# Kernel optimization log

Measured on AMD Instinct MI355X. Metric: run time of the kernel, lower is better.

Reference implementation:

```python
import jax, jax.numpy as jnp
import numpy as np

N = 50000       # nodes per batched graph
E = 800000      # edges per batched graph
G = 256         # graphs per batch (for max-node pooling)
VOCAB = 120     # node types == embedding vocab
D_EMB = 32
D_H = 100
D_FC = 32
MIN_TYPE = 5    # min_type_count in compute_node_pair_mmd
CAP = 25        # max_nodes_per_type (deterministic: first CAP nodes per type)
KER_MUL = 2.0   # standard multi-kernel Gaussian MMD settings
KER_NUM = 5


def setup_inputs() -> dict:
    key = jax.random.key(0)
    ks = jax.random.split(key, 16)
    ri = lambda k, sh, hi: jax.random.randint(k, sh, 0, hi, dtype=jnp.int32)
    feat = ri(ks[0], (N,), VOCAB)
    feat_src = ri(ks[1], (N,), VOCAB)
    feat_tar = ri(ks[2], (N,), VOCAB)
    edge_index = ri(ks[3], (2, E), N)
    edge_index_src = ri(ks[4], (2, E), N)
    edge_index_tar = ri(ks[5], (2, E), N)
    graph_ids = (jnp.arange(N, dtype=jnp.int32) * G) // N  # sorted, even partition
    mask = (jax.random.uniform(ks[6], (N,)) > 0.1).astype(jnp.float32)
    embed = jax.random.normal(ks[7], (VOCAB, D_EMB)) * 0.02
    gcn_w = jax.random.normal(ks[8], (D_EMB, D_H)) * (1.0 / np.sqrt(D_EMB))
    gcn_b = jnp.zeros((D_H,), jnp.float32)
    fc_w = jax.random.normal(ks[9], (D_H, D_FC)) * (1.0 / np.sqrt(D_H))
    fc_b = jnp.zeros((D_FC,), jnp.float32)
    def_w = jax.random.normal(ks[10], (D_FC, 1)) * (1.0 / np.sqrt(D_FC))
    def_b = jnp.zeros((1,), jnp.float32)
    return dict(feat=feat, feat_src=feat_src, feat_tar=feat_tar,
                edge_index=edge_index, edge_index_src=edge_index_src,
                edge_index_tar=edge_index_tar, graph_ids=graph_ids, mask=mask,
                embed=embed, gcn_w=gcn_w, gcn_b=gcn_b, fc_w=fc_w, fc_b=fc_b,
                def_w=def_w, def_b=def_b)


def _graph_conv(x, ei, w, b):
    # DGL GraphConv, norm='both': D_out^{-1/2} A^T D_in^{-1/2} X W + b (degrees clamped to 1)
    src, dst = ei[0], ei[1]
    ones = jnp.ones((ei.shape[1],), x.dtype)
    outdeg = jnp.clip(jax.ops.segment_sum(ones, src, num_segments=N), 1.0)
    indeg = jnp.clip(jax.ops.segment_sum(ones, dst, num_segments=N), 1.0)
    h = (x @ w) * (outdeg ** -0.5)[:, None]          # [N, D_H], weight first (in<=out)
    agg = jax.ops.segment_sum(h[src], dst, num_segments=N)
    return agg * (indeg ** -0.5)[:, None] + b


def _mmd(src_types, tgt_types, src_feats, tgt_feats):
    # per-type multi-kernel Gaussian MMD; deterministic cap of CAP nodes/type
    def per_type(t):
        sm = (src_types == t)
        tm = (tgt_types == t)
        s_cnt = sm.sum()
        t_cnt = tm.sum()
        sv, si = jax.lax.top_k(sm.astype(jnp.float32), CAP)  # first CAP indices of type t
        tv, ti = jax.lax.top_k(tm.astype(jnp.float32), CAP)
        X = jnp.concatenate([src_feats[si], tgt_feats[ti]], 0)      # [2C, D]
        valid = jnp.concatenate([sv, tv]) > 0                        # [2C]
        pm = valid[:, None] & valid[None, :]
        D2 = jnp.sum((X[:, None, :] - X[None, :, :]) ** 2, -1)      # [2C, 2C]
        m = jnp.minimum(s_cnt, CAP).astype(jnp.float32)
        n = jnp.minimum(t_cnt, CAP).astype(jnp.float32)
        ntot = m + n
        bw = jnp.sum(jnp.where(pm, D2, 0.0)) / jnp.maximum(ntot * ntot - ntot, 1.0)
        bw = bw / (KER_MUL ** (KER_NUM // 2))
        bws = bw * (KER_MUL ** jnp.arange(KER_NUM, dtype=jnp.float32))
        K = jnp.sum(jnp.exp(-D2[None] / jnp.maximum(bws, 1e-8)[:, None, None]), 0)
        K = jnp.where(pm, K, 0.0)
        XX = K[:CAP, :CAP].sum() / jnp.maximum(m * m, 1.0)
        YY = K[CAP:, CAP:].sum() / jnp.maximum(n * n, 1.0)
        XY = K[:CAP, CAP:].sum() / jnp.maximum(m * n, 1.0)
        loss = XX + YY - 2.0 * XY
        inc = (s_cnt >= MIN_TYPE) & (t_cnt >= MIN_TYPE)
        return jnp.where(inc, loss, 0.0), inc.astype(jnp.float32)
    losses, incs = jax.vmap(per_type)(jnp.arange(1, VOCAB, dtype=jnp.int32))  # type 0 skipped
    cnt = incs.sum()
    return jnp.where(cnt > 0, losses.sum() / jnp.maximum(cnt, 1.0), 0.0)


def reference(feat, feat_src, feat_tar, edge_index, edge_index_src, edge_index_tar,
              graph_ids, mask, embed, gcn_w, gcn_b, fc_w, fc_b, def_w, def_b):
    def process(f, ei, msk):
        x = embed[f]
        if msk is not None:
            x = x * msk[:, None]
        h = jax.nn.relu(_graph_conv(x, ei, gcn_w, gcn_b))            # node feats 'h'
        pooled = jax.ops.segment_max(h, graph_ids, num_segments=G,
                                     indices_are_sorted=True)        # dgl.max_nodes
        return h, pooled

    _, pool = process(feat, edge_index, mask)
    h_src, pool_src = process(feat_src, edge_index_src, None)
    h_tar, pool_tar = process(feat_tar, edge_index_tar, None)

    x_batch_mmd = pool @ fc_w + fc_b        # [G, 32]
    x_src_mmd = pool_src @ fc_w + fc_b
    x_tar_mmd = pool_tar @ fc_w + fc_b
    src_node_feat = h_src @ fc_w + fc_b     # [N, 32]
    tgt_node_feat = h_tar @ fc_w + fc_b
    x_loss_mmd_node = _mmd(feat_src, feat_tar, src_node_feat, tgt_node_feat)
    defect_prob = jax.nn.sigmoid(x_batch_mmd @ def_w + def_b)  # [G, 1]
    # domain_clf output is not returned by the original forward, so it is skipped here.
    return (x_batch_mmd, defect_prob, x_src_mmd, x_tar_mmd, x_loss_mmd_node)
```

## Files before the change

### kernel.cpp

```cpp
#include <hip/hip_runtime.h>
#include <hip/hip_bf16.h>

#define Nn 50000
#define Ee 800000
#define Gg 256
#define VOC 120
#define DH 100
#define CAPc 25
#define NTYPE 119
#define NCHUNK 196
#define DR 4
#define DS 32
#define DWORDS 6250
#define NBIN 391
#define EBLK 782

#define P1_T 0
#define P1_SEL 120
#define P1_BIN 512
#define P1_DEG 2858
#define P1_PCLR 3242
#define P1_SCLR 3317
#define P1_TOT 3415
#define P3_SELG 0
#define P3_BSC 392
#define P3_DMG 2738
#define P3_TOT 3031

__global__ __launch_bounds__(256) void prep_kernel(
        const float* __restrict__ embed, const float* __restrict__ gcn_w, float* __restrict__ Tp,
        const int* __restrict__ feat_src, const int* __restrict__ feat_tar,
        int* __restrict__ chunkcnt,
        const int* __restrict__ ei0, const int* __restrict__ ei1, const int* __restrict__ ei2,
        int* __restrict__ cntbuf, int* __restrict__ partial,
        float* __restrict__ pool, int* __restrict__ selpos) {
    __shared__ int sm[DWORDS];
    int bx = blockIdx.x;
    int tid = threadIdx.x;

    if (bx < P1_SEL) {
        int t = bx - P1_T;
        if (tid < DH) {
            float acc = 0.f;
#pragma unroll
            for (int k = 0; k < 32; ++k) acc = fmaf(embed[t * 32 + k], gcn_w[k * DH + tid], acc);
            Tp[t * DH + tid] = acc;
        }
        return;
    }
    if (bx < P1_BIN) {
        int idx = bx - P1_SEL;
        int side = idx / NCHUNK, chunk = idx - side * NCHUNK;
        const int* f = side ? feat_tar : feat_src;
        if (tid < VOC) sm[tid] = 0;
        __syncthreads();
        int i = chunk * 256 + tid;
        if (i < Nn) atomicAdd(&sm[f[i]], 1);
        __syncthreads();
        if (tid < VOC) chunkcnt[(side * NCHUNK + chunk) * VOC + tid] = sm[tid];
        return;
    }
    if (bx < P1_DEG) {
        int idx = bx - P1_BIN;
        int g = idx / EBLK, blk = idx - g * EBLK;
        const int* dst = ((g == 0) ? ei0 : (g == 1) ? ei1 : ei2) + Ee;
        for (int i = tid; i < NBIN; i += 256) sm[i] = 0;
        __syncthreads();
        int e0 = (blk * 256 + tid) * 4;
        if (e0 < Ee) {
            uint4 d = *(const uint4*)&dst[e0];
            atomicAdd(&sm[d.x >> 7], 1);
            atomicAdd(&sm[d.y >> 7], 1);
            atomicAdd(&sm[d.z >> 7], 1);
            atomicAdd(&sm[d.w >> 7], 1);
        }
        __syncthreads();
        for (int i = tid; i < NBIN; i += 256)
            cntbuf[((size_t)g * NBIN + i) * EBLK + blk] = sm[i];
        return;
    }
    if (bx < P1_PCLR) {
        int idx = bx - P1_DEG;
        int g = idx / (DR * DS), rs = idx - g * (DR * DS);
        int r = rs & (DR - 1), s = rs >> 2;
        const int* ei = (g == 0) ? ei0 : (g == 1) ? ei1 : ei2;
        const uint4* a4 = (const uint4*)(ei + s * (Ee / DS));
        for (int i = tid; i < DWORDS; i += 256) sm[i] = 0;
        __syncthreads();
        unsigned base = r * (2 * DWORDS);
        for (int idx2 = tid; idx2 < (Ee / DS) / 4; idx2 += 256) {
            uint4 v = a4[idx2];
            unsigned q;
            q = v.x - base; if (q < 2 * DWORDS) atomicAdd(&sm[q >> 1], 1 << ((q & 1) * 16));
            q = v.y - base; if (q < 2 * DWORDS) atomicAdd(&sm[q >> 1], 1 << ((q & 1) * 16));
            q = v.z - base; if (q < 2 * DWORDS) atomicAdd(&sm[q >> 1], 1 << ((q & 1) * 16));
            q = v.w - base; if (q < 2 * DWORDS) atomicAdd(&sm[q >> 1], 1 << ((q & 1) * 16));
        }
        __syncthreads();
        int* outp = partial + ((size_t)(g * DR + r) * DS + s) * DWORDS;
        for (int i = tid; i < DWORDS; i += 256) outp[i] = sm[i];
        return;
    }
    if (bx < P1_SCLR) {
        int i = (bx - P1_PCLR) * 256 + tid;
        ((float4*)pool)[i] = make_float4(0.f, 0.f, 0.f, 0.f);
        return;
    }
    {
        int i = (bx - P1_SCLR) * 256 + tid;
        if (i < 25000) ((int4*)selpos)[i] = make_int4(-1, -1, -1, -1);
        return;
    }
}

__global__ __launch_bounds__(64) void prefix_kernel(const int* __restrict__ chunkcnt,
                                                    int* __restrict__ baseb,
                                                    int* __restrict__ fullcnt,
                                                    const int* __restrict__ cntbuf,
                                                    int* __restrict__ ofsbuf,
                                                    int* __restrict__ bintot) {
    int bx = blockIdx.x;
    int lane = threadIdx.x;
    if (bx < 2 * VOC) {
        int side = bx / VOC, t = bx - side * VOC;
        int run = 0;
        for (int c0 = 0; c0 < NCHUNK; c0 += 64) {
            int c = c0 + lane;
            int v = (c < NCHUNK) ? chunkcnt[(side * NCHUNK + c) * VOC + t] : 0;
            int inc = v;
#pragma unroll
            for (int o = 1; o < 64; o <<= 1) {
                int u = __shfl_up(inc, o, 64);
                if (lane >= o) inc += u;
            }
            if (c < NCHUNK) baseb[(side * NCHUNK + c) * VOC + t] = run + inc - v;
            run += __shfl(inc, 63, 64);
        }
        if (lane == 0) fullcnt[side * VOC + t] = run;
    } else {
        int pair = bx - 2 * VOC;
        const int* src = cntbuf + (size_t)pair * EBLK;
        int* dst = ofsbuf + (size_t)pair * EBLK;
        int run = 0;
        for (int c0 = 0; c0 < EBLK; c0 += 64) {
            int c = c0 + lane;
            int v = (c < EBLK) ? src[c] : 0;
            int inc = v;
#pragma unroll
            for (int o = 1; o < 64; o <<= 1) {
                int u = __shfl_up(inc, o, 64);
                if (lane >= o) inc += u;
            }
            if (c < EBLK) dst[c] = run + inc - v;
            run += __shfl(inc, 63, 64);
        }
        if (lane == 0) bintot[pair] = run;
    }
}

__global__ __launch_bounds__(64) void binbase_kernel(const int* __restrict__ bintot,
                                                     int* __restrict__ binbase) {
    int g = blockIdx.x;
    int lane = threadIdx.x;
    int run = 0;
    for (int c0 = 0; c0 < NBIN; c0 += 64) {
        int c = c0 + lane;
        int v = (c < NBIN) ? bintot[g * NBIN + c] : 0;
        int inc = v;
#pragma unroll
        for (int o = 1; o < 64; o <<= 1) {
            int u = __shfl_up(inc, o, 64);
            if (lane >= o) inc += u;
        }
        if (c < NBIN) binbase[g * NBIN + c] = run + inc - v;
        run += __shfl(inc, 63, 64);
    }
}

__global__ __launch_bounds__(256) void scatter_kernel(
        const int* __restrict__ feat_src, const int* __restrict__ feat_tar,
        const int* __restrict__ baseb, int* __restrict__ selpos_src, int* __restrict__ selpos_tar,
        const int* __restrict__ ei0, const int* __restrict__ ei1, const int* __restrict__ ei2,
        const int* __restrict__ ofsbuf, const int* __restrict__ binbase,
        unsigned* __restrict__ ebuf,
        const int* __restrict__ partial, const int* __restrict__ feat0,
        const float* __restrict__ mask, float2* __restrict__ pc) {
    __shared__ int sm[NBIN];
    int bx = blockIdx.x;
    int tid = threadIdx.x;

    if (bx < P3_BSC) {
        int idx = bx - P3_SELG;
        int side = idx / NCHUNK, chunk = idx - side * NCHUNK;
        const int* f = side ? feat_tar : feat_src;
        int* selpos = side ? selpos_tar : selpos_src;
        int i = chunk * 256 + tid;
        int t = (i < Nn) ? f[i] : -1;
        sm[tid] = t;
        int bv = 0;
        bool need = (t >= 1);
        if (need) {
            bv = baseb[(side * NCHUNK + chunk) * VOC + t];
            need = (bv < CAPc);
        }
        int any = __syncthreads_count((int)need);
        if (any == 0) return;
        if (need) {
            int rank = bv;
            for (int q = 0; q < 256; ++q)
                if (q < tid && sm[q] == t) rank++;
            if (rank < CAPc) selpos[i] = (t - 1) * CAPc + rank;
        }
        return;
    }
    if (bx < P3_DMG) {
        int idx = bx - P3_BSC;
        int g = idx / EBLK, blk = idx - g * EBLK;
        const int* ei = (g == 0) ? ei0 : (g == 1) ? ei1 : ei2;
        for (int i = tid; i < NBIN; i += 256)
            sm[i] = binbase[g * NBIN + i] + ofsbuf[((size_t)g * NBIN + i) * EBLK + blk];
        __syncthreads();
        unsigned* eb = ebuf + (size_t)g * Ee;
        int e0 = (blk * 256 + tid) * 4;
        if (e0 < Ee) {
            uint4 s = *(const uint4*)&ei[e0];
            uint4 d = *(const uint4*)&ei[Ee + e0];
            int p;
            p = atomicAdd(&sm[d.x >> 7], 1); eb[p] = ((d.x & 127u) << 16) | s.x;
            p = atomicAdd(&sm[d.y >> 7], 1); eb[p] = ((d.y & 127u) << 16) | s.y;
            p = atomicAdd(&sm[d.z >> 7], 1); eb[p] = ((d.z & 127u) << 16) | s.z;
            p = atomicAdd(&sm[d.w >> 7], 1); eb[p] = ((d.w & 127u) << 16) | s.w;
        }
        return;
    }
    {
        int idx = (bx - P3_DMG) * 256 + tid;
        if (idx >= 3 * DR * DWORDS) return;
        int g = idx / (DR * DWORDS);
        int rem = idx - g * (DR * DWORDS);
        int r = rem / DWORDS, w = rem - r * DWORDS;
        const int* p = partial + ((size_t)(g * DR + r) * DS) * DWORDS + w;
        int sum = 0;
#pragma unroll 8
        for (int s = 0; s < DS; ++s) sum += p[s * DWORDS];
        int c0 = sum & 0xFFFF, c1 = sum >> 16;
        int n0 = r * (2 * DWORDS) + 2 * w;
        const int* ft = (g == 0) ? feat0 : (g == 1) ? feat_src : feat_tar;
        float cf0 = rsqrtf((float)max(c0, 1));
        float cf1 = rsqrtf((float)max(c1, 1));
        if (g == 0) {
            cf0 *= mask[n0];
            cf1 *= mask[n0 + 1];
        }
        float4 v = make_float4(cf0, __int_as_float(ft[n0]), cf1, __int_as_float(ft[n0 + 1]));
        ((float4*)(pc + (size_t)g * Nn))[r * DWORDS + w] = v;
        return;
    }
}

__global__ __launch_bounds__(256, 2) void fused_wh_kernel(const unsigned* __restrict__ ebuf,
                                                          const float2* __restrict__ pc,
                                                          const int* __restrict__ binbase,
                                                          const int* __restrict__ bintot,
                                                          const float* __restrict__ Tp,
                                                          const int* __restrict__ selposall,
                                                          float* __restrict__ h_sel,
                                                          const float* __restrict__ gcn_b,
                                                          float* __restrict__ pool) {
    __shared__ float Wl[VOC * 128];
    __shared__ int cnt[128];
    int g = blockIdx.y, bin = blockIdx.x;
    int tid = threadIdx.x;

    float4* Wl4 = (float4*)Wl;
#pragma unroll
    for (int i = 0; i < 15; ++i) Wl4[tid + i * 256] = make_float4(0.f, 0.f, 0.f, 0.f);
    if (tid < 128) cnt[tid] = 0;
    __syncthreads();

    int base = binbase[g * NBIN + bin];
    int n = bintot[g * NBIN + bin];
    const unsigned* eb = ebuf + (size_t)g * Ee + base;
    const float2* pcg = pc + (size_t)g * Nn;
    for (int i = tid; i < n; i += 256) {
        unsigned e = eb[i];
        float2 p = pcg[e & 0xFFFFu];
        int dl = e >> 16;
        atomicAdd(&Wl[__float_as_int(p.y) * 128 + dl], p.x);
        atomicAdd(&cnt[dl], 1);
    }
    __syncthreads();

    int lane = tid & 63, wv = tid >> 6;
    int chcol = __builtin_amdgcn_readfirstlane(wv) * 25;
    const float* Tc = Tp + chcol;
    int r0 = bin * 128;
    int nr = min(128, Nn - r0);
    float accA[25], accB[25];
#pragma unroll
    for (int j = 0; j < 25; ++j) { accA[j] = 0.f; accB[j] = 0.f; }

    for (int t0 = 0; t0 < VOC; t0 += 8) {
        float wA8[8], wB8[8];
#pragma unroll
        for (int u = 0; u < 8; ++u) {
            wA8[u] = Wl[(t0 + u) * 128 + lane];
            wB8[u] = Wl[(t0 + u) * 128 + lane + 64];
        }
#pragma unroll
        for (int u = 0; u < 8; ++u) {
            const float* tr = Tc + (t0 + u) * DH;
#pragma unroll
            for (int j = 0; j < 25; ++j) {
                float tv = tr[j];
                accA[j] = fmaf(wA8[u], tv, accA[j]);
                accB[j] = fmaf(wB8[u], tv, accB[j]);
            }
        }
    }

    int rA = lane, rB = lane + 64;
    bool vA = rA < nr, vB = rB < nr;
    float rsA = vA ? rsqrtf((float)max(cnt[rA], 1)) : 0.f;
    float rsB = vB ? rsqrtf((float)max(cnt[rB], 1)) : 0.f;
    int growA = r0 + rA, growB = r0 + rB;
    int seg0 = (r0 * Gg) / Nn;
    int segA = (growA * Gg) / Nn, segB = (growB * Gg) / Nn;
    float bb[25];
#pragma unroll
    for (int j = 0; j < 25; ++j) bb[j] = gcn_b[wv * 25 + j];

    float v0[25], v1[25];
#pragma unroll
    for (int j = 0; j < 25; ++j) {
        float hA = vA ? fmaxf(fmaf(accA[j], rsA, bb[j]), 0.f) : 0.f;
        float hB = vB ? fmaxf(fmaf(accB[j], rsB, bb[j]), 0.f) : 0.f;
        accA[j] = hA;
        accB[j] = hB;
        v0[j] = fmaxf((vA && segA == seg0) ? hA : 0.f, (vB && segB == seg0) ? hB : 0.f);
        v1[j] = fmaxf((vA && segA != seg0) ? hA : 0.f, (vB && segB != seg0) ? hB : 0.f);
    }
#pragma unroll
    for (int m = 1; m < 64; m <<= 1) {
#pragma unroll
        for (int j = 0; j < 25; ++j) {
            v0[j] = fmaxf(v0[j], __shfl_xor(v0[j], m, 64));
            v1[j] = fmaxf(v1[j], __shfl_xor(v1[j], m, 64));
        }
    }
    if (lane == 0) {
        float* poolg = pool + g * (Gg * DH) + seg0 * DH + wv * 25;
        for (int j = 0; j < 25; ++j) atomicMax((int*)&poolg[j], __float_as_int(v0[j]));
        int segLast = ((r0 + nr - 1) * Gg) / Nn;
        if (segLast != seg0)
            for (int j = 0; j < 25; ++j) atomicMax((int*)&poolg[DH + j], __float_as_int(v1[j]));
    }

    if (g > 0) {
        const int* selpos = selposall + (size_t)(g - 1) * Nn;
        float* hs = h_sel + (size_t)(g == 2 ? NTYPE * CAPc * DH : 0);
        int spA = vA ? selpos[growA] : -1;
        int spB = vB ? selpos[growB] : -1;
        if (spA >= 0) {
            float* d = hs + (size_t)spA * DH + wv * 25;
            for (int j = 0; j < 25; ++j) d[j] = accA[j];
        }
        if (spB >= 0) {
            float* d = hs + (size_t)spB * DH + wv * 25;
            for (int j = 0; j < 25; ++j) d[j] = accB[j];
        }
    }
}

__global__ __launch_bounds__(256) void post_kernel(const float* __restrict__ pool,
                                                   const float* __restrict__ fc_w,
                                                   const float* __restrict__ fc_b,
                                                   const float* __restrict__ def_w,
                                                   const float* __restrict__ def_b,
                                                   float* __restrict__ out,
                                                   const float* __restrict__ h_sel,
                                                   const int* __restrict__ fullcnt,
                                                   float* __restrict__ X) {
    __shared__ float smf[DH * 32];
    int bx = blockIdx.x;
    int tid = threadIdx.x;
    if (bx < Gg) {
        int g = bx;
        if (tid < 96) {
            int p = tid >> 5, j = tid & 31;
            float acc = fc_b[j];
            const float* pr = pool + p * (Gg * DH) + g * DH;
#pragma unroll 4
            for (int k = 0; k < DH; ++k) acc = fmaf(pr[k], fc_w[k * 32 + j], acc);
            int off = (p == 0) ? 0 : (p == 1 ? 8448 : 16640);
            out[off + g * 32 + j] = acc;
            if (p == 0) smf[j] = acc;
        }
        __syncthreads();
        if (tid < 32) {
            float v = smf[tid] * def_w[tid];
            for (int o = 16; o; o >>= 1) v += __shfl_down(v, o, 64);
            if (tid == 0) out[8192 + g] = 1.f / (1.f + expf(-(v + def_b[0])));
        }
        return;
    }
    {
        int t = bx - Gg;
        for (int i = tid; i < DH * 32; i += 256) smf[i] = fc_w[i];
        __syncthreads();
        int cs = min(fullcnt[t + 1], CAPc);
        int ct = min(fullcnt[VOC + t + 1], CAPc);
        int j = tid & 31, rg = tid >> 5;
        for (int r = rg; r < 2 * CAPc; r += 8) {
            int side = r / CAPc, rr = r % CAPc;
            int cnt = side ? ct : cs;
            float acc = 0.f;
            if (rr < cnt) {
                const float* hr = h_sel + ((size_t)side * NTYPE * CAPc + (size_t)t * CAPc + rr) * DH;
                acc = fc_b[j];
#pragma unroll 4
                for (int k = 0; k < DH; ++k) acc = fmaf(hr[k], smf[k * 32 + j], acc);
            }
            X[(size_t)t * 1600 + r * 32 + j] = acc;
        }
        return;
    }
}

__device__ __forceinline__ float block_reduce256(float v, float* red, int tid) {
    __syncthreads();
    red[tid] = v;
    __syncthreads();
    for (int s = 128; s > 0; s >>= 1) {
        if (tid < s) red[tid] += red[tid + s];
        __syncthreads();
    }
    return red[0];
}

__global__ __launch_bounds__(256) void mmd_kernel(const float* __restrict__ X,
                                                  const int* __restrict__ fullcnt,
                                                  float* __restrict__ losses) {
    int t = blockIdx.x;
    __shared__ float Xs[50 * 32];
    __shared__ float D2[50 * 50];
    __shared__ float red[256];
    int tid = threadIdx.x;
    for (int i = tid; i < 1600; i += 256) Xs[i] = X[(size_t)t * 1600 + i];
    __syncthreads();
    int scF = fullcnt[t + 1];
    int tcF = fullcnt[VOC + t + 1];
    int m = min(scF, CAPc), n2 = min(tcF, CAPc);
    float bwpart = 0.f;
    for (int idx = tid; idx < 2500; idx += 256) {
        int i = idx / 50, j = idx % 50;
        float d = 0.f;
#pragma unroll
        for (int k = 0; k < 32; ++k) {
            float df = Xs[i * 32 + k] - Xs[j * 32 + k];
            d = fmaf(df, df, d);
        }
        D2[idx] = d;
        bool vi = (i < CAPc) ? (i < m) : (i - CAPc < n2);
        bool vj = (j < CAPc) ? (j < m) : (j - CAPc < n2);
        if (vi && vj) bwpart += d;
    }
    float bwsum = block_reduce256(bwpart, red, tid);
    float ntot = (float)(m + n2);
    float bw = bwsum / fmaxf(ntot * ntot - ntot, 1.f) * 0.25f;
    float bws[5];
#pragma unroll
    for (int k = 0; k < 5; ++k) bws[k] = fmaxf(bw * (float)(1 << k), 1e-8f);
    float xx = 0.f, yy = 0.f, xy = 0.f;
    for (int idx = tid; idx < 2500; idx += 256) {
        int i = idx / 50, j = idx % 50;
        bool vi = (i < CAPc) ? (i < m) : (i - CAPc < n2);
        bool vj = (j < CAPc) ? (j < m) : (j - CAPc < n2);
        if (!(vi && vj)) continue;
        float d = D2[idx];
        float kv = 0.f;
#pragma unroll
        for (int k = 0; k < 5; ++k) kv += expf(-d / bws[k]);
        if (i < CAPc && j < CAPc) xx += kv;
        else if (i >= CAPc && j >= CAPc) yy += kv;
        else if (i < CAPc) xy += kv;
    }
    float rxx = block_reduce256(xx, red, tid);
    float ryy = block_reduce256(yy, red, tid);
    float rxy = block_reduce256(xy, red, tid);
    if (tid == 0) {
        float fm = (float)m, fn = (float)n2;
        float XX = rxx / fmaxf(fm * fm, 1.f);
        float YY = ryy / fmaxf(fn * fn, 1.f);
        float XY = rxy / fmaxf(fm * fn, 1.f);
        float loss = XX + YY - 2.f * XY;
        int inc = (scF >= 5 && tcF >= 5) ? 1 : 0;
        losses[t * 2 + 0] = inc ? loss : 0.f;
        losses[t * 2 + 1] = (float)inc;
    }
}

__global__ void final_kernel(const float* __restrict__ losses, float* __restrict__ out) {
    __shared__ float red[128], redc[128];
    int tid = threadIdx.x;
    float s = 0.f, c = 0.f;
    for (int t = tid; t < NTYPE; t += 128) {
        s += losses[t * 2];
        c += losses[t * 2 + 1];
    }
    red[tid] = s;
    redc[tid] = c;
    __syncthreads();
    for (int st = 64; st > 0; st >>= 1) {
        if (tid < st) {
            red[tid] += red[tid + st];
            redc[tid] += redc[tid + st];
        }
        __syncthreads();
    }
    if (tid == 0) out[24832] = redc[0] > 0.f ? red[0] / fmaxf(redc[0], 1.f) : 0.f;
}

extern "C" void kernel_launch(void* const* d_in, const int* in_sizes, int n_in,
                              void* d_out, int out_size, void* d_ws, size_t ws_size,
                              hipStream_t stream) {
    const int* feat = (const int*)d_in[0];
    const int* feat_src = (const int*)d_in[1];
    const int* feat_tar = (const int*)d_in[2];
    const int* ei0 = (const int*)d_in[3];
    const int* ei1 = (const int*)d_in[4];
    const int* ei2 = (const int*)d_in[5];
    const float* mask = (const float*)d_in[7];
    const float* embed = (const float*)d_in[8];
    const float* gcn_w = (const float*)d_in[9];
    const float* gcn_b = (const float*)d_in[10];
    const float* fc_w = (const float*)d_in[11];
    const float* fc_b = (const float*)d_in[12];
    const float* def_w = (const float*)d_in[13];
    const float* def_b = (const float*)d_in[14];
    float* out = (float*)d_out;

    char* wsb = (char*)d_ws;
    int* partial = (int*)(wsb + 0);
    float* Tp = (float*)(wsb + 9600000);
    float* pool = (float*)(wsb + 9660000);
    float2* pc = (float2*)(wsb + 9967200);
    int* selpos = (int*)(wsb + 11167200);
    float* h_sel = (float*)(wsb + 11567200);
    int* fullcnt = (int*)(wsb + 13947200);
    float* X = (float*)(wsb + 13948160);
    float* losses = (float*)(wsb + 14709760);
    int* chunkcnt = (int*)(wsb + 14710720);
    int* baseb = (int*)(wsb + 14898880);
    int* cntbuf = (int*)(wsb + 15087040);
    int* ofsbuf = (int*)(wsb + 18756200);
    int* bintot = (int*)(wsb + 22425400);
    int* binbase = (int*)(wsb + 22430400);
    unsigned* ebuf = (unsigned*)(wsb + 22435200);

    prep_kernel<<<P1_TOT, 256, 0, stream>>>(embed, gcn_w, Tp, feat_src, feat_tar, chunkcnt,
                                            ei0, ei1, ei2, cntbuf, partial, pool, selpos);
    prefix_kernel<<<2 * VOC + 3 * NBIN, 64, 0, stream>>>(chunkcnt, baseb, fullcnt, cntbuf,
                                                         ofsbuf, bintot);
    binbase_kernel<<<3, 64, 0, stream>>>(bintot, binbase);
    scatter_kernel<<<P3_TOT, 256, 0, stream>>>(feat_src, feat_tar, baseb, selpos, selpos + Nn,
                                               ei0, ei1, ei2, ofsbuf, binbase, ebuf, partial,
                                               feat, mask, pc);
    fused_wh_kernel<<<dim3(NBIN, 3), 256, 0, stream>>>(ebuf, pc, binbase, bintot, Tp, selpos,
                                                       h_sel, gcn_b, pool);
    post_kernel<<<Gg + NTYPE, 256, 0, stream>>>(pool, fc_w, fc_b, def_w, def_b, out, h_sel,
                                                fullcnt, X);
    mmd_kernel<<<NTYPE, 256, 0, stream>>>(X, fullcnt, losses);
    final_kernel<<<1, 128, 0, stream>>>(losses, out);
}
```

Measured before the change: 215.0 us.

## Transpose bin-count layout, fold final reduction into mmd kernel, raise wave priority

The per-block bin counts and offsets are now stored block-major instead of bin-major. Each histogram and scatter block therefore writes and reads a contiguous row, while the prefix kernel reads strided. The separate final reduction kernel is dropped: mmd blocks atomically add loss and count into a stats buffer, and the last-finishing block writes the mean, which saves one launch. The main accumulation loop in fused_wh is also wrapped in s_setprio. The float atomic sum makes the result order nondeterministic.

```diff
diff --git a/kernel.cpp b/kernel.cpp
--- a/kernel.cpp
+++ b/kernel.cpp
@@ -33,7 +33,7 @@
         int* __restrict__ chunkcnt,
         const int* __restrict__ ei0, const int* __restrict__ ei1, const int* __restrict__ ei2,
         int* __restrict__ cntbuf, int* __restrict__ partial,
-        float* __restrict__ pool, int* __restrict__ selpos) {
+        float* __restrict__ pool, int* __restrict__ selpos, float* __restrict__ stats) {
     __shared__ int sm[DWORDS];
     int bx = blockIdx.x;
     int tid = threadIdx.x;
@@ -75,8 +75,8 @@
             atomicAdd(&sm[d.w >> 7], 1);
         }
         __syncthreads();
-        for (int i = tid; i < NBIN; i += 256)
-            cntbuf[((size_t)g * NBIN + i) * EBLK + blk] = sm[i];
+        int* outp = cntbuf + ((size_t)blk * 3 + g) * NBIN;
+        for (int i = tid; i < NBIN; i += 256) outp[i] = sm[i];
         return;
     }
     if (bx < P1_PCLR) {
@@ -107,8 +107,14 @@
         return;
     }
     {
-        int i = (bx - P1_SCLR) * 256 + tid;
+        int b = bx - P1_SCLR;
+        int i = b * 256 + tid;
         if (i < 25000) ((int4*)selpos)[i] = make_int4(-1, -1, -1, -1);
+        if (b == 0 && tid == 0) {
+            stats[0] = 0.f;
+            ((int*)stats)[1] = 0;
+            ((int*)stats)[2] = 0;
+        }
         return;
     }
 }
@@ -139,19 +145,18 @@
         if (lane == 0) fullcnt[side * VOC + t] = run;
     } else {
         int pair = bx - 2 * VOC;
-        const int* src = cntbuf + (size_t)pair * EBLK;
-        int* dst = ofsbuf + (size_t)pair * EBLK;
+        int g = pair / NBIN, bin = pair - g * NBIN;
         int run = 0;
         for (int c0 = 0; c0 < EBLK; c0 += 64) {
             int c = c0 + lane;
-            int v = (c < EBLK) ? src[c] : 0;
+            int v = (c < EBLK) ? cntbuf[((size_t)c * 3 + g) * NBIN + bin] : 0;
             int inc = v;
 #pragma unroll
             for (int o = 1; o < 64; o <<= 1) {
                 int u = __shfl_up(inc, o, 64);
                 if (lane >= o) inc += u;
             }
-            if (c < EBLK) dst[c] = run + inc - v;
+            if (c < EBLK) ofsbuf[((size_t)c * 3 + g) * NBIN + bin] = run + inc - v;
             run += __shfl(inc, 63, 64);
         }
         if (lane == 0) bintot[pair] = run;
@@ -217,8 +222,9 @@
         int idx = bx - P3_BSC;
         int g = idx / EBLK, blk = idx - g * EBLK;
         const int* ei = (g == 0) ? ei0 : (g == 1) ? ei1 : ei2;
+        const int* ofp = ofsbuf + ((size_t)blk * 3 + g) * NBIN;
         for (int i = tid; i < NBIN; i += 256)
-            sm[i] = binbase[g * NBIN + i] + ofsbuf[((size_t)g * NBIN + i) * EBLK + blk];
+            sm[i] = binbase[g * NBIN + i] + ofp[i];
         __syncthreads();
         unsigned* eb = ebuf + (size_t)g * Ee;
         int e0 = (blk * 256 + tid) * 4;
@@ -300,6 +306,7 @@
 #pragma unroll
     for (int j = 0; j < 25; ++j) { accA[j] = 0.f; accB[j] = 0.f; }
 
+    __builtin_amdgcn_s_setprio(1);
     for (int t0 = 0; t0 < VOC; t0 += 8) {
         float wA8[8], wB8[8];
 #pragma unroll
@@ -318,6 +325,7 @@
             }
         }
     }
+    __builtin_amdgcn_s_setprio(0);
 
     int rA = lane, rB = lane + 64;
     bool vA = rA < nr, vB = rB < nr;
@@ -440,7 +448,8 @@
 
 __global__ __launch_bounds__(256) void mmd_kernel(const float* __restrict__ X,
                                                   const int* __restrict__ fullcnt,
-                                                  float* __restrict__ losses) {
+                                                  float* __restrict__ stats,
+                                                  float* __restrict__ out) {
     int t = blockIdx.x;
     __shared__ float Xs[50 * 32];
     __shared__ float D2[50 * 50];
@@ -495,30 +504,16 @@
         float XY = rxy / fmaxf(fm * fn, 1.f);
         float loss = XX + YY - 2.f * XY;
         int inc = (scF >= 5 && tcF >= 5) ? 1 : 0;
-        losses[t * 2 + 0] = inc ? loss : 0.f;
-        losses[t * 2 + 1] = (float)inc;
-    }
-}
-
-__global__ void final_kernel(const float* __restrict__ losses, float* __restrict__ out) {
-    __shared__ float red[128], redc[128];
-    int tid = threadIdx.x;
-    float s = 0.f, c = 0.f;
-    for (int t = tid; t < NTYPE; t += 128) {
-        s += losses[t * 2];
-        c += losses[t * 2 + 1];
-    }
-    red[tid] = s;
-    redc[tid] = c;
-    __syncthreads();
-    for (int st = 64; st > 0; st >>= 1) {
-        if (tid < st) {
-            red[tid] += red[tid + st];
-            redc[tid] += redc[tid + st];
-        }
-        __syncthreads();
-    }
-    if (tid == 0) out[24832] = redc[0] > 0.f ? red[0] / fmaxf(redc[0], 1.f) : 0.f;
+        atomicAdd(&stats[0], inc ? loss : 0.f);
+        atomicAdd((int*)&stats[1], inc);
+        __threadfence();
+        int old = atomicAdd((int*)&stats[2], 1);
+        if (old == NTYPE - 1) {
+            float s = atomicAdd(&stats[0], 0.f);
+            int c = atomicAdd((int*)&stats[1], 0);
+            out[24832] = (c > 0) ? s / (float)max(c, 1) : 0.f;
+        }
+    }
 }
 
 extern "C" void kernel_launch(void* const* d_in, const int* in_sizes, int n_in,
@@ -549,7 +544,7 @@
     float* h_sel = (float*)(wsb + 11567200);
     int* fullcnt = (int*)(wsb + 13947200);
     float* X = (float*)(wsb + 13948160);
-    float* losses = (float*)(wsb + 14709760);
+    float* stats = (float*)(wsb + 14709760);
     int* chunkcnt = (int*)(wsb + 14710720);
     int* baseb = (int*)(wsb + 14898880);
     int* cntbuf = (int*)(wsb + 15087040);
@@ -559,7 +554,7 @@
     unsigned* ebuf = (unsigned*)(wsb + 22435200);
 
     prep_kernel<<<P1_TOT, 256, 0, stream>>>(embed, gcn_w, Tp, feat_src, feat_tar, chunkcnt,
-                                            ei0, ei1, ei2, cntbuf, partial, pool, selpos);
+                                            ei0, ei1, ei2, cntbuf, partial, pool, selpos, stats);
     prefix_kernel<<<2 * VOC + 3 * NBIN, 64, 0, stream>>>(chunkcnt, baseb, fullcnt, cntbuf,
                                                          ofsbuf, bintot);
     binbase_kernel<<<3, 64, 0, stream>>>(bintot, binbase);
@@ -570,6 +565,5 @@
                                                        h_sel, gcn_b, pool);
     post_kernel<<<Gg + NTYPE, 256, 0, stream>>>(pool, fc_w, fc_b, def_w, def_b, out, h_sel,
                                                 fullcnt, X);
-    mmd_kernel<<<NTYPE, 256, 0, stream>>>(X, fullcnt, losses);
-    final_kernel<<<1, 128, 0, stream>>>(losses, out);
-}
+    mmd_kernel<<<NTYPE, 256, 0, stream>>>(X, fullcnt, stats, out);
+}
```

After: 214.4 us. No clear change (-0.3%).
